# Optimization experiments

Measured on AMD Instinct MI355X. Metric: run time of the kernel, lower is better.

Reference implementation:

```python
import jax, jax.numpy as jnp
import numpy as np
import math


def _packet_loss_to_partial_patch(x, loss_rate):
    # Zero out randomly-chosen 1472-byte chunks of the NHWC-flattened tensor,
    # exactly mirroring the torch loop but as one vectorized masked multiply.
    B, C, H, W = x.shape
    xp = jnp.transpose(x, (0, 2, 3, 1)).reshape(-1)  # NHWC flatten
    n = xp.shape[0]
    elem_size = 4  # float32 bytes
    elems_per_chunk = 1472 // elem_size  # 368
    num_chunks = math.ceil(n * elem_size / 1472)
    num_lossy = int(math.ceil(num_chunks * (loss_rate / 100)))
    perm = jax.random.permutation(jax.random.key(1234), num_chunks)
    keep = jnp.ones((num_chunks,), xp.dtype).at[perm[:num_lossy]].set(0.0)
    elem_keep = jnp.repeat(keep, elems_per_chunk)[:n]
    xp = xp * elem_keep
    return jnp.transpose(xp.reshape(B, H, W, C), (0, 3, 1, 2))


def setup_inputs() -> dict:
    key = jax.random.key(0)
    ks = jax.random.split(key, 7)
    B, C, H, W = 32, 256, 56, 56
    r = 16
    s = 0.05
    return {
        "x": jax.random.normal(ks[0], (B, C, H, W), jnp.float32),
        "fc1_w": jax.random.normal(ks[1], (C // r, C), jnp.float32) * s,
        "fc2_w": jax.random.normal(ks[2], (C, C // r), jnp.float32) * s,
        "threshold": jnp.array([0.5], jnp.float32),
        "detect_w": jax.random.normal(ks[3], (C, C), jnp.float32) * s,
        "rec1_w": jax.random.normal(ks[4], (C, 2 * C), jnp.float32) * s,
        "rec2_w": jax.random.normal(ks[5], (C, C), jnp.float32) * s,
        "adapt_w": jax.random.normal(ks[6], (C, 1), jnp.float32) * s,
        "Packet_Loss_Rate": 50,
    }


def reference(x, fc1_w, fc2_w, threshold, detect_w, rec1_w, rec2_w, adapt_w, Packet_Loss_Rate):
    x = _packet_loss_to_partial_patch(x, Packet_Loss_Rate)
    B, C, H, W = x.shape
    # SE channel attention
    y = jnp.mean(x, axis=(2, 3))                              # [B, C]
    scores = jax.nn.sigmoid(jax.nn.relu(y @ fc1_w.T) @ fc2_w.T)  # [B, C]
    # packet-loss adaptation: Linear(1 -> C) applied to rate*ones([B,1])
    adapt = jnp.asarray(Packet_Loss_Rate, x.dtype) * adapt_w[:, 0]  # [C]
    mask = jax.nn.relu(scores + adapt[None, :] - threshold)   # [B, C]
    mask = mask[:, :, None, None]
    # 1x1 convs as channel GEMMs
    det = jnp.einsum('oc,bchw->bohw', detect_w, x)
    z = jnp.concatenate([x, jax.nn.sigmoid(det) * x], axis=1)  # [B, 2C, H, W]
    r = jax.nn.relu(jnp.einsum('oc,bchw->bohw', rec1_w, z))
    r = jnp.einsum('oc,bchw->bohw', rec2_w, r)
    return r * mask
```

## Files before the change

### kernel.cpp

```cpp
#include <hip/hip_runtime.h>
#include <stdint.h>

#define PARTITIONABLE 1

typedef float f32x4 __attribute__((ext_vector_type(4)));
typedef short bf16x8 __attribute__((ext_vector_type(8)));

namespace {
constexpr int Hh = 56, Ww = 56;
constexpr int HW = Hh * Ww;
constexpr int Bsz = 32, Cch = 256;
constexpr int NCH = 69811;
constexpr int HALF = 34906;
constexpr int NB2 = 4096;

constexpr int SC1_W   = 0;
constexpr int SC2_W   = 139648;
constexpr int BITS1_W = 279296;
constexpr int BITS2_W = 349120;
constexpr int R1_W    = 418944;
constexpr int R2_W    = 488768;
constexpr int HIST1_W = 558592;
constexpr int PRE1_W  = 562688;
constexpr int CNT1_W  = 566784;
constexpr int HIST2_W = 570880;
constexpr int PRE2_W  = 574976;
constexpr int CNT2_W  = 579072;
constexpr int Y_W     = 583168;

constexpr int KEEP_W  = 0;
constexpr int MASKV_W = 69824;
constexpr int WPACK_W = 78016;
}

__host__ __device__ constexpr uint32_t rotl32(uint32_t v, int r) {
  return (v << r) | (v >> (32 - r));
}
__host__ __device__ constexpr uint64_t tf2x32(uint32_t k0, uint32_t k1,
                                              uint32_t x0, uint32_t x1) {
  uint32_t ks2 = k0 ^ k1 ^ 0x1BD11BDAu;
  x0 += k0; x1 += k1;
  {const int R[4]={13,15,26,6};  for(int i=0;i<4;i++){x0+=x1;x1=rotl32(x1,R[i]);x1^=x0;}}
  x0 += k1;  x1 += ks2 + 1u;
  {const int R[4]={17,29,16,24}; for(int i=0;i<4;i++){x0+=x1;x1=rotl32(x1,R[i]);x1^=x0;}}
  x0 += ks2; x1 += k0 + 2u;
  {const int R[4]={13,15,26,6};  for(int i=0;i<4;i++){x0+=x1;x1=rotl32(x1,R[i]);x1^=x0;}}
  x0 += k0;  x1 += k1 + 3u;
  {const int R[4]={17,29,16,24}; for(int i=0;i<4;i++){x0+=x1;x1=rotl32(x1,R[i]);x1^=x0;}}
  x0 += k1;  x1 += ks2 + 4u;
  {const int R[4]={13,15,26,6};  for(int i=0;i<4;i++){x0+=x1;x1=rotl32(x1,R[i]);x1^=x0;}}
  x0 += ks2; x1 += k0 + 5u;
  return ((uint64_t)x0 << 32) | x1;
}

#if PARTITIONABLE
constexpr uint64_t KEY1 = tf2x32(0u, 1234u, 0u, 0u);
constexpr uint64_t SUB1 = tf2x32(0u, 1234u, 0u, 1u);
constexpr uint64_t SUB2 = tf2x32((uint32_t)(KEY1 >> 32), (uint32_t)KEY1, 0u, 1u);
constexpr uint32_t S1H = (uint32_t)(SUB1 >> 32), S1L = (uint32_t)SUB1;
constexpr uint32_t S2H = (uint32_t)(SUB2 >> 32), S2L = (uint32_t)SUB2;
#else
constexpr uint64_t E0 = tf2x32(0u, 1234u, 0u, 2u);
constexpr uint64_t E1 = tf2x32(0u, 1234u, 1u, 3u);
constexpr uint32_t K1H = (uint32_t)(E0 >> 32), K1L = (uint32_t)(E1 >> 32);
constexpr uint64_t F0 = tf2x32(K1H, K1L, 0u, 2u);
constexpr uint64_t F1 = tf2x32(K1H, K1L, 1u, 3u);
constexpr uint32_t S1H = (uint32_t)E0, S1L = (uint32_t)E1;
constexpr uint32_t S2H = (uint32_t)F0, S2L = (uint32_t)F1;
#endif

__device__ __forceinline__ uint32_t rnd_bits(uint32_t kh, uint32_t kl, uint32_t i) {
#if PARTITIONABLE
  uint64_t r = tf2x32(kh, kl, 0u, i);
  return (uint32_t)(r >> 32) ^ (uint32_t)r;
#else
  if (i < (uint32_t)HALF) {
    uint32_t x1 = (i + HALF < (uint32_t)NCH) ? i + HALF : 0u;
    return (uint32_t)(tf2x32(kh, kl, i, x1) >> 32);
  } else {
    return (uint32_t)tf2x32(kh, kl, i - HALF, i);
  }
#endif
}

__device__ __forceinline__ uint32_t f2bf(float f) {
  uint32_t u = __float_as_uint(f);
  return (u + 0x7FFFu + ((u >> 16) & 1u)) >> 16;
}
__device__ __forceinline__ float bf2f(uint32_t h) {
  return __uint_as_float(h << 16);
}
__device__ __forceinline__ uint32_t cvtpk(float lo, float hi) {
  uint32_t r;
  asm("v_cvt_pk_bf16_f32 %0, %1, %2" : "=v"(r) : "v"(lo), "v"(hi));
  return r;
}

__global__ void k_bits(uint32_t* bits1, uint32_t* bits2,
                       uint32_t* hist1, uint32_t* hist2) {
  int i = blockIdx.x * 256 + threadIdx.x;
  if (i >= NCH) return;
  uint32_t b1 = rnd_bits(S1H, S1L, (uint32_t)i);
  uint32_t b2 = rnd_bits(S2H, S2L, (uint32_t)i);
  bits1[i] = b1; bits2[i] = b2;
  atomicAdd(&hist1[b1 >> 20], 1u);
  atomicAdd(&hist2[b2 >> 20], 1u);
}

__global__ __launch_bounds__(1024) void k_scan2(const uint32_t* h1, uint32_t* p1o,
                                                const uint32_t* h2, uint32_t* p2o) {
  const uint32_t* h = blockIdx.x ? h2 : h1;
  uint32_t* pre = blockIdx.x ? p2o : p1o;
  __shared__ uint32_t part[1024];
  int t = threadIdx.x;
  uint4 v = *(const uint4*)&h[t * 4];
  uint32_t s = v.x + v.y + v.z + v.w;
  part[t] = s;
  __syncthreads();
  for (int off = 1; off < 1024; off <<= 1) {
    uint32_t u = (t >= off) ? part[t - off] : 0u;
    __syncthreads();
    part[t] += u;
    __syncthreads();
  }
  uint32_t run = part[t] - s;
  uint4 o;
  o.x = run; o.y = run + v.x; o.z = o.y + v.y; o.w = o.z + v.z;
  *(uint4*)&pre[t * 4] = o;
}

__global__ void k_scatter2(const uint32_t* bits1, const uint32_t* pre1,
                           uint32_t* cnt1, uint64_t* sc1,
                           const uint32_t* bits2, const uint32_t* pre2,
                           uint32_t* cnt2, uint64_t* sc2) {
  int blk = blockIdx.x;
  bool second = blk >= 273;
  const uint32_t* bits = second ? bits2 : bits1;
  const uint32_t* pre  = second ? pre2  : pre1;
  uint32_t* cnt = second ? cnt2 : cnt1;
  uint64_t* sc  = second ? sc2  : sc1;
  int i = (second ? blk - 273 : blk) * 256 + threadIdx.x;
  if (i >= NCH) return;
  uint32_t b = bits[i], bk = b >> 20;
  uint32_t pos = pre[bk] + atomicAdd(&cnt[bk], 1u);
  sc[pos] = ((uint64_t)b << 32) | (uint32_t)i;
}

__global__ void k_rank2(const uint32_t* bits1, const uint32_t* pre1,
                        const uint32_t* hist1, const uint64_t* sc1, uint32_t* rk1,
                        const uint32_t* bits2, const uint32_t* pre2,
                        const uint32_t* hist2, const uint64_t* sc2, uint32_t* rk2) {
  int blk = blockIdx.x;
  bool second = blk >= 273;
  const uint32_t* bits = second ? bits2 : bits1;
  const uint32_t* pre  = second ? pre2  : pre1;
  const uint32_t* hist = second ? hist2 : hist1;
  const uint64_t* sc   = second ? sc2   : sc1;
  uint32_t* rnk = second ? rk2 : rk1;
  int i = (second ? blk - 273 : blk) * 256 + threadIdx.x;
  if (i >= NCH) return;
  uint32_t b = bits[i], bk = b >> 20;
  uint32_t s = pre[bk], n = hist[bk];
  uint64_t my = ((uint64_t)b << 32) | (uint32_t)i;
  uint32_t c = 0;
  for (uint32_t k = 0; k < n; ++k) c += (sc[s + k] < my) ? 1u : 0u;
  rnk[i] = s + c;
}

__global__ void k_keepwpack(const uint32_t* r1, const uint32_t* r2,
                            const int* plr, float* keep,
                            const float* __restrict__ dw,
                            const float* __restrict__ r1w,
                            const float* __restrict__ r2w,
                            ushort* __restrict__ wdp, ushort* __restrict__ w1p,
                            ushort* __restrict__ w2p) {
  int blk = blockIdx.x;
  if (blk < 273) {
    int j = blk * 256 + threadIdx.x;
    if (j >= NCH) return;
    int L = (NCH * plr[0] + 99) / 100;
    keep[j] = (r2[r1[j]] < (uint32_t)L) ? 0.f : 1.f;
    return;
  }
  int tid = (blk - 273) * 256 + threadIdx.x;
  const float* src;
  ushort* dst;
  if (tid < 8192) {
    int s = tid, ot = s >> 9, ks = (s >> 6) & 7, l = s & 63;
    src = dw + (ot * 16 + (l & 15)) * 256 + ks * 32 + (l >> 4) * 8;
    dst = wdp + s * 8;
  } else if (tid < 24576) {
    int s = tid - 8192, ot = s >> 10, ks = (s >> 6) & 15, l = s & 63;
    src = r1w + (ot * 16 + (l & 15)) * 512 + ks * 32 + (l >> 4) * 8;
    dst = w1p + s * 8;
  } else {
    int s = tid - 24576, ot = s >> 9, ks = (s >> 6) & 7, l = s & 63;
    src = r2w + (ot * 16 + (l & 15)) * 256 + ks * 32 + (l >> 4) * 8;
    dst = w2p + s * 8;
  }
  float4 v0 = *(const float4*)src;
  float4 v1 = *(const float4*)(src + 4);
  uint4 pk;
  pk.x = f2bf(v0.x) | (f2bf(v0.y) << 16);
  pk.y = f2bf(v0.z) | (f2bf(v0.w) << 16);
  pk.z = f2bf(v1.x) | (f2bf(v1.y) << 16);
  pk.w = f2bf(v1.z) | (f2bf(v1.w) << 16);
  *(uint4*)dst = pk;
}

__global__ void k_ymean(const float* __restrict__ x, const float* __restrict__ keep,
                        float* __restrict__ y) {
  int bc = blockIdx.x;
  int b = bc >> 8, c = bc & 255;
  const float4* row = (const float4*)(x + (size_t)bc * HW);
  int t = threadIdx.x;
  float s = 0.f;
  for (int q = t; q < HW / 4; q += 256) {
    float4 v = row[q];
    uint32_t base = (uint32_t)((b * HW + q * 4) * 256 + c);
    s += v.x * keep[base / 368u];
    s += v.y * keep[(base + 256u) / 368u];
    s += v.z * keep[(base + 512u) / 368u];
    s += v.w * keep[(base + 768u) / 368u];
  }
  for (int off = 32; off > 0; off >>= 1) s += __shfl_down(s, off);
  __shared__ float w4[4];
  if ((t & 63) == 0) w4[t >> 6] = s;
  __syncthreads();
  if (t == 0) y[bc] = (w4[0] + w4[1] + w4[2] + w4[3]) * (1.0f / HW);
}

__global__ void k_scores(const float* __restrict__ y, const float* __restrict__ fc1,
                         const float* __restrict__ fc2, const float* __restrict__ thr,
                         const float* __restrict__ aw, const int* __restrict__ plr,
                         float* __restrict__ maskv) {
  int b = blockIdx.x, t = threadIdx.x;
  __shared__ float ysh[256];
  __shared__ float hsh[16];
  ysh[t] = y[b * 256 + t];
  __syncthreads();
  if (t < 16) {
    float a = 0.f;
    for (int c = 0; c < 256; ++c) a += ysh[c] * fc1[t * 256 + c];
    hsh[t] = fmaxf(a, 0.f);
  }
  __syncthreads();
  float s = 0.f;
  #pragma unroll
  for (int j = 0; j < 16; ++j) s += hsh[j] * fc2[t * 16 + j];
  float sc = 1.f / (1.f + expf(-s));
  float m = sc + (float)plr[0] * aw[t] - thr[0];
  maskv[b * 256 + t] = fmaxf(m, 0.f);
}

__global__ __launch_bounds__(1024, 8) void k_main(
    const float* __restrict__ x, const float* __restrict__ keep,
    const ushort* __restrict__ wdp, const ushort* __restrict__ w1p,
    const ushort* __restrict__ w2p, const float* __restrict__ maskv,
    float* __restrict__ out) {
  __shared__ __align__(16) short SM[32768];
  int tile = blockIdx.x;
  int bb = tile / 49, hw0 = (tile % 49) * 64;
  int t = threadIdx.x;
  int lane = t & 63, w = t >> 6;
  int l15 = lane & 15, lhi = lane >> 4;

  {
    const float* xb = x + (size_t)bb * (Cch * HW);
    uint32_t pixb = (uint32_t)(bb * HW + hw0);
    int p = lane;
    uint32_t ia0 = (pixb + (uint32_t)p) * 256u;
    uint32_t k0 = ia0 / 368u;
    uint32_t cstar = 368u * (k0 + 1u) - ia0;
    float kp0 = keep[k0];
    float kp1 = keep[k0 + 1];
    const float* xcol = xb + hw0 + p;
    int ks = w >> 1;
    #pragma unroll
    for (int k2 = 0; k2 < 2; ++k2) {
      int k = (w & 1) * 2 + k2;
      int cb = ks * 32 + k * 8;
      uint32_t pw[4];
      #pragma unroll
      for (int h = 0; h < 4; ++h) {
        uint32_t ca = (uint32_t)(cb + h * 2);
        float va = xcol[(size_t)ca * HW] * (ca < cstar ? kp0 : kp1);
        float vb = xcol[(size_t)(ca + 1u) * HW] * ((ca + 1u) < cstar ? kp0 : kp1);
        pw[h] = cvtpk(va, vb);
      }
      uint4 pk; pk.x = pw[0]; pk.y = pw[1]; pk.z = pw[2]; pk.w = pw[3];
      *(uint4*)&SM[(ks * 4 + (p >> 4)) * 512 + ((p & 15) + 16 * k) * 8] = pk;
    }
  }
  __syncthreads();

  f32x4 zero4 = {0.f, 0.f, 0.f, 0.f};
  f32x4 acc[4];
  int stoff = ((w >> 1) * 4) * 512 +
              (l15 + 16 * ((w & 1) * 2 + (lhi >> 1))) * 8 + (lhi & 1) * 4;

  #pragma unroll
  for (int nt = 0; nt < 4; ++nt) acc[nt] = zero4;
  {
    const ushort* ap = wdp + (w * 8) * 512 + lane * 8;
    bf16x8 a0 = *(const bf16x8*)ap;
    #pragma unroll
    for (int ks = 0; ks < 8; ++ks) {
      bf16x8 na0 = a0;
      if (ks < 7) na0 = *(const bf16x8*)(ap + (ks + 1) * 512);
      #pragma unroll
      for (int nt = 0; nt < 4; ++nt) {
        bf16x8 b = *(const bf16x8*)&SM[(ks * 4 + nt) * 512 + lane * 8];
        acc[nt] = __builtin_amdgcn_mfma_f32_16x16x32_bf16(a0, b, acc[nt], 0, 0, 0);
      }
      a0 = na0;
    }
  }

  #pragma unroll
  for (int nt = 0; nt < 4; ++nt) {
    int off = stoff + nt * 512;
    ushort4 xv = *(const ushort4*)&SM[off];
    float s0 = bf2f(xv.x) / (1.f + __expf(-acc[nt][0]));
    float s1 = bf2f(xv.y) / (1.f + __expf(-acc[nt][1]));
    float s2 = bf2f(xv.z) / (1.f + __expf(-acc[nt][2]));
    float s3 = bf2f(xv.w) / (1.f + __expf(-acc[nt][3]));
    uint2 sv;
    sv.x = cvtpk(s0, s1);
    sv.y = cvtpk(s2, s3);
    *(uint2*)&SM[16384 + off] = sv;
  }
  __syncthreads();

  f32x4 acc2[4];
  #pragma unroll
  for (int nt = 0; nt < 4; ++nt) acc2[nt] = zero4;
  {
    const ushort* ap = w1p + (w * 16) * 512 + lane * 8;
    bf16x8 a0 = *(const bf16x8*)ap;
    #pragma unroll
    for (int ks = 0; ks < 16; ++ks) {
      bf16x8 na0 = a0;
      if (ks < 15) na0 = *(const bf16x8*)(ap + (ks + 1) * 512);
      #pragma unroll
      for (int nt = 0; nt < 4; ++nt) {
        bf16x8 b = *(const bf16x8*)&SM[(ks * 4 + nt) * 512 + lane * 8];
        acc2[nt] = __builtin_amdgcn_mfma_f32_16x16x32_bf16(a0, b, acc2[nt], 0, 0, 0);
      }
      a0 = na0;
    }
  }
  __syncthreads();

  #pragma unroll
  for (int nt = 0; nt < 4; ++nt) {
    int off = stoff + nt * 512;
    uint2 rv;
    rv.x = cvtpk(fmaxf(acc2[nt][0], 0.f), fmaxf(acc2[nt][1], 0.f));
    rv.y = cvtpk(fmaxf(acc2[nt][2], 0.f), fmaxf(acc2[nt][3], 0.f));
    *(uint2*)&SM[off] = rv;
  }
  __syncthreads();

  #pragma unroll
  for (int nt = 0; nt < 4; ++nt) acc[nt] = zero4;
  {
    const ushort* ap = w2p + (w * 8) * 512 + lane * 8;
    bf16x8 a0 = *(const bf16x8*)ap;
    #pragma unroll
    for (int ks = 0; ks < 8; ++ks) {
      bf16x8 na0 = a0;
      if (ks < 7) na0 = *(const bf16x8*)(ap + (ks + 1) * 512);
      #pragma unroll
      for (int nt = 0; nt < 4; ++nt) {
        bf16x8 b = *(const bf16x8*)&SM[(ks * 4 + nt) * 512 + lane * 8];
        acc[nt] = __builtin_amdgcn_mfma_f32_16x16x32_bf16(a0, b, acc[nt], 0, 0, 0);
      }
      a0 = na0;
    }
  }
  __syncthreads();

  {
    float* EP = (float*)SM;
    int sw = ((lhi & 1) << 2) | ((lhi >> 1) << 4);
    #pragma unroll
    for (int r = 0; r < 4; ++r) {
      int c = w * 16 + 4 * lhi + r;
      float m = maskv[bb * 256 + c];
      #pragma unroll
      for (int nt = 0; nt < 4; ++nt)
        EP[c * 64 + ((nt * 16 + l15) ^ sw)] = acc[nt][r] * m;
    }
  }
  __syncthreads();
  {
    const float* EP = (const float*)SM;
    float* op = out + (size_t)bb * (Cch * HW) + hw0;
    #pragma unroll
    for (int q = 0; q < 4; ++q) {
      int idx4 = q * 1024 + t;
      int c = idx4 >> 4;
      int colw = (idx4 & 15) * 4;
      int p = colw ^ ((((c >> 2) & 1) << 2) | (((c >> 3) & 1) << 4));
      f32x4 v = *(const f32x4*)&EP[idx4 * 4];
      *(f32x4*)(op + (size_t)c * HW + p) = v;
    }
  }
}

extern "C" void kernel_launch(void* const* d_in, const int* in_sizes, int n_in,
                              void* d_out, int out_size, void* d_ws, size_t ws_size,
                              hipStream_t stream) {
  const float* x   = (const float*)d_in[0];
  const float* fc1 = (const float*)d_in[1];
  const float* fc2 = (const float*)d_in[2];
  const float* thr = (const float*)d_in[3];
  const float* dw  = (const float*)d_in[4];
  const float* r1w = (const float*)d_in[5];
  const float* r2w = (const float*)d_in[6];
  const float* aw  = (const float*)d_in[7];
  const int*   plr = (const int*)d_in[8];

  float*    out = (float*)d_out;
  uint32_t* ob  = (uint32_t*)d_out;
  float*    ws  = (float*)d_ws;

  uint64_t* sc1   = (uint64_t*)(ob + SC1_W);
  uint64_t* sc2   = (uint64_t*)(ob + SC2_W);
  uint32_t* bits1 = ob + BITS1_W;
  uint32_t* bits2 = ob + BITS2_W;
  uint32_t* r1    = ob + R1_W;
  uint32_t* r2    = ob + R2_W;
  uint32_t* hist1 = ob + HIST1_W;
  uint32_t* pre1  = ob + PRE1_W;
  uint32_t* cnt1  = ob + CNT1_W;
  uint32_t* hist2 = ob + HIST2_W;
  uint32_t* pre2  = ob + PRE2_W;
  uint32_t* cnt2  = ob + CNT2_W;
  float*    yv    = (float*)(ob + Y_W);

  float*  keep  = ws + KEEP_W;
  float*  maskv = ws + MASKV_W;
  ushort* wdp   = (ushort*)(ws + WPACK_W);
  ushort* w1p   = wdp + 65536;
  ushort* w2p   = w1p + 131072;

  hipMemsetAsync((void*)(ob + HIST1_W), 0, (size_t)6 * NB2 * 4, stream);

  dim3 blk(256);
  k_bits<<<273, blk, 0, stream>>>(bits1, bits2, hist1, hist2);
  k_scan2<<<2, 1024, 0, stream>>>(hist1, pre1, hist2, pre2);
  k_scatter2<<<546, blk, 0, stream>>>(bits1, pre1, cnt1, sc1,
                                      bits2, pre2, cnt2, sc2);
  k_rank2<<<546, blk, 0, stream>>>(bits1, pre1, hist1, sc1, r1,
                                   bits2, pre2, hist2, sc2, r2);
  k_keepwpack<<<401, blk, 0, stream>>>(r1, r2, plr, keep, dw, r1w, r2w,
                                       wdp, w1p, w2p);
  k_ymean<<<8192, blk, 0, stream>>>(x, keep, yv);
  k_scores<<<32, blk, 0, stream>>>(yv, fc1, fc2, thr, aw, plr, maskv);
  k_main<<<1568, 1024, 0, stream>>>(x, keep, wdp, w1p, w2p, maskv, out);
}
```

Measured before the change: 158.5 us.

## Switch fused GEMM chain to 32x32x16 MFMA with 256-thread blocks

Repacks the three weight matrices for the 32x32x16 bf16 MFMA layout and rewrites the main kernel so each of 4 waves computes a 64-channel by 64-pixel tile as 2x2 32x32 MFMA blocks, instead of 16 waves each doing 16x16 tiles. Fewer waves load more weight fragments each and reuse every LDS B fragment across two MFMAs. The aim is higher arithmetic per LDS read and less weight traffic per block. In exchange each wave holds far more accumulator registers, so occupancy and latency hiding drop. The epilogue also loses its LDS swizzle, which can add bank conflicts.

Result: slower. 178.3 us (+12.5%).

```diff
diff --git a/kernel.cpp b/kernel.cpp
--- a/kernel.cpp
+++ b/kernel.cpp
@@ -4,6 +4,7 @@
 #define PARTITIONABLE 1
 
 typedef float f32x4 __attribute__((ext_vector_type(4)));
+typedef float f32x16 __attribute__((ext_vector_type(16)));
 typedef short bf16x8 __attribute__((ext_vector_type(8)));
 
 namespace {
@@ -186,16 +187,16 @@
   const float* src;
   ushort* dst;
   if (tid < 8192) {
-    int s = tid, ot = s >> 9, ks = (s >> 6) & 7, l = s & 63;
-    src = dw + (ot * 16 + (l & 15)) * 256 + ks * 32 + (l >> 4) * 8;
+    int s = tid, ct = s >> 10, ks = (s >> 6) & 15, l = s & 63;
+    src = dw + (ct * 32 + (l & 31)) * 256 + ks * 16 + (l >> 5) * 8;
     dst = wdp + s * 8;
   } else if (tid < 24576) {
-    int s = tid - 8192, ot = s >> 10, ks = (s >> 6) & 15, l = s & 63;
-    src = r1w + (ot * 16 + (l & 15)) * 512 + ks * 32 + (l >> 4) * 8;
+    int s = tid - 8192, ct = s >> 11, ks = (s >> 6) & 31, l = s & 63;
+    src = r1w + (ct * 32 + (l & 31)) * 512 + ks * 16 + (l >> 5) * 8;
     dst = w1p + s * 8;
   } else {
-    int s = tid - 24576, ot = s >> 9, ks = (s >> 6) & 7, l = s & 63;
-    src = r2w + (ot * 16 + (l & 15)) * 256 + ks * 32 + (l >> 4) * 8;
+    int s = tid - 24576, ct = s >> 10, ks = (s >> 6) & 15, l = s & 63;
+    src = r2w + (ct * 32 + (l & 31)) * 256 + ks * 16 + (l >> 5) * 8;
     dst = w2p + s * 8;
   }
   float4 v0 = *(const float4*)src;
@@ -253,7 +254,7 @@
   maskv[b * 256 + t] = fmaxf(m, 0.f);
 }
 
-__global__ __launch_bounds__(1024, 8) void k_main(
+__global__ __launch_bounds__(256, 2) void k_main(
     const float* __restrict__ x, const float* __restrict__ keep,
     const ushort* __restrict__ wdp, const ushort* __restrict__ w1p,
     const ushort* __restrict__ w2p, const float* __restrict__ maskv,
@@ -263,134 +264,175 @@
   int bb = tile / 49, hw0 = (tile % 49) * 64;
   int t = threadIdx.x;
   int lane = t & 63, w = t >> 6;
-  int l15 = lane & 15, lhi = lane >> 4;
+  int l31 = lane & 31, lhi = lane >> 5;
 
   {
-    const float* xb = x + (size_t)bb * (Cch * HW);
-    uint32_t pixb = (uint32_t)(bb * HW + hw0);
-    int p = lane;
-    uint32_t ia0 = (pixb + (uint32_t)p) * 256u;
+    int px = t & 63;
+    uint32_t ia0 = (uint32_t)(bb * HW + hw0 + px) * 256u;
     uint32_t k0 = ia0 / 368u;
     uint32_t cstar = 368u * (k0 + 1u) - ia0;
-    float kp0 = keep[k0];
-    float kp1 = keep[k0 + 1];
-    const float* xcol = xb + hw0 + p;
-    int ks = w >> 1;
-    #pragma unroll
-    for (int k2 = 0; k2 < 2; ++k2) {
-      int k = (w & 1) * 2 + k2;
-      int cb = ks * 32 + k * 8;
+    float kp0 = keep[k0], kp1 = keep[k0 + 1];
+    const float* xcol = x + (size_t)bb * (Cch * HW) + hw0 + px;
+    int g0 = t >> 6;
+    int nt = px >> 5;
+    float xr[8][8];
+    #pragma unroll
+    for (int gi = 0; gi < 8; ++gi) {
+      int cb = g0 * 8 + gi * 32;
+      #pragma unroll
+      for (int h = 0; h < 8; ++h)
+        xr[gi][h] = xcol[(size_t)(cb + h) * HW];
+    }
+    #pragma unroll
+    for (int gi = 0; gi < 8; ++gi) {
+      int G = g0 + gi * 4;
+      int cb = G * 8;
       uint32_t pw[4];
       #pragma unroll
       for (int h = 0; h < 4; ++h) {
-        uint32_t ca = (uint32_t)(cb + h * 2);
-        float va = xcol[(size_t)ca * HW] * (ca < cstar ? kp0 : kp1);
-        float vb = xcol[(size_t)(ca + 1u) * HW] * ((ca + 1u) < cstar ? kp0 : kp1);
+        uint32_t ca = (uint32_t)(cb + 2 * h);
+        float va = xr[gi][2 * h]     * (ca < cstar ? kp0 : kp1);
+        float vb = xr[gi][2 * h + 1] * ((ca + 1u) < cstar ? kp0 : kp1);
         pw[h] = cvtpk(va, vb);
       }
       uint4 pk; pk.x = pw[0]; pk.y = pw[1]; pk.z = pw[2]; pk.w = pw[3];
-      *(uint4*)&SM[(ks * 4 + (p >> 4)) * 512 + ((p & 15) + 16 * k) * 8] = pk;
-    }
-  }
-  __syncthreads();
-
-  f32x4 zero4 = {0.f, 0.f, 0.f, 0.f};
-  f32x4 acc[4];
-  int stoff = ((w >> 1) * 4) * 512 +
-              (l15 + 16 * ((w & 1) * 2 + (lhi >> 1))) * 8 + (lhi & 1) * 4;
+      int ks = G >> 1, half = G & 1;
+      *(uint4*)&SM[(((ks * 2 + nt) * 64) + half * 32 + (px & 31)) * 8] = pk;
+    }
+  }
+  __syncthreads();
+
+  const f32x16 z16 = {0.f};
+  f32x16 acc[2][2];
+
+  acc[0][0] = z16; acc[0][1] = z16; acc[1][0] = z16; acc[1][1] = z16;
+  {
+    const ushort* a0p = wdp + (size_t)(w * 2 + 0) * 16 * 512 + lane * 8;
+    const ushort* a1p = a0p + 16 * 512;
+    bf16x8 a0 = *(const bf16x8*)a0p;
+    bf16x8 a1 = *(const bf16x8*)a1p;
+    #pragma unroll
+    for (int ks = 0; ks < 16; ++ks) {
+      bf16x8 na0 = a0, na1 = a1;
+      if (ks < 15) {
+        na0 = *(const bf16x8*)(a0p + (ks + 1) * 512);
+        na1 = *(const bf16x8*)(a1p + (ks + 1) * 512);
+      }
+      #pragma unroll
+      for (int nt = 0; nt < 2; ++nt) {
+        bf16x8 b = *(const bf16x8*)&SM[(ks * 2 + nt) * 512 + lane * 8];
+        acc[0][nt] = __builtin_amdgcn_mfma_f32_32x32x16_bf16(a0, b, acc[0][nt], 0, 0, 0);
+        acc[1][nt] = __builtin_amdgcn_mfma_f32_32x32x16_bf16(a1, b, acc[1][nt], 0, 0, 0);
+      }
+      a0 = na0; a1 = na1;
+    }
+  }
 
   #pragma unroll
-  for (int nt = 0; nt < 4; ++nt) acc[nt] = zero4;
+  for (int tc = 0; tc < 2; ++tc) {
+    #pragma unroll
+    for (int q = 0; q < 4; ++q) {
+      int ksp = (w * 2 + tc) * 2 + (q >> 1);
+      int dl = ((q & 1) << 5) | l31;
+      #pragma unroll
+      for (int nt = 0; nt < 2; ++nt) {
+        int base = (ksp * 2 + nt) * 512 + dl * 8 + lhi * 4;
+        ushort4 xv = *(const ushort4*)&SM[base];
+        float e0 = bf2f(xv.x) / (1.f + __expf(-acc[tc][nt][4 * q + 0]));
+        float e1 = bf2f(xv.y) / (1.f + __expf(-acc[tc][nt][4 * q + 1]));
+        float e2 = bf2f(xv.z) / (1.f + __expf(-acc[tc][nt][4 * q + 2]));
+        float e3 = bf2f(xv.w) / (1.f + __expf(-acc[tc][nt][4 * q + 3]));
+        uint2 sv;
+        sv.x = cvtpk(e0, e1);
+        sv.y = cvtpk(e2, e3);
+        *(uint2*)&SM[16384 + base] = sv;
+      }
+    }
+  }
+  __syncthreads();
+
+  f32x16 acc2[2][2];
+  acc2[0][0] = z16; acc2[0][1] = z16; acc2[1][0] = z16; acc2[1][1] = z16;
   {
-    const ushort* ap = wdp + (w * 8) * 512 + lane * 8;
-    bf16x8 a0 = *(const bf16x8*)ap;
-    #pragma unroll
-    for (int ks = 0; ks < 8; ++ks) {
-      bf16x8 na0 = a0;
-      if (ks < 7) na0 = *(const bf16x8*)(ap + (ks + 1) * 512);
-      #pragma unroll
-      for (int nt = 0; nt < 4; ++nt) {
-        bf16x8 b = *(const bf16x8*)&SM[(ks * 4 + nt) * 512 + lane * 8];
-        acc[nt] = __builtin_amdgcn_mfma_f32_16x16x32_bf16(a0, b, acc[nt], 0, 0, 0);
-      }
-      a0 = na0;
-    }
-  }
+    const ushort* a0p = w1p + (size_t)(w * 2 + 0) * 32 * 512 + lane * 8;
+    const ushort* a1p = a0p + 32 * 512;
+    bf16x8 a0 = *(const bf16x8*)a0p;
+    bf16x8 a1 = *(const bf16x8*)a1p;
+    #pragma unroll
+    for (int ks = 0; ks < 32; ++ks) {
+      bf16x8 na0 = a0, na1 = a1;
+      if (ks < 31) {
+        na0 = *(const bf16x8*)(a0p + (ks + 1) * 512);
+        na1 = *(const bf16x8*)(a1p + (ks + 1) * 512);
+      }
+      #pragma unroll
+      for (int nt = 0; nt < 2; ++nt) {
+        bf16x8 b = *(const bf16x8*)&SM[(ks * 2 + nt) * 512 + lane * 8];
+        acc2[0][nt] = __builtin_amdgcn_mfma_f32_32x32x16_bf16(a0, b, acc2[0][nt], 0, 0, 0);
+        acc2[1][nt] = __builtin_amdgcn_mfma_f32_32x32x16_bf16(a1, b, acc2[1][nt], 0, 0, 0);
+      }
+      a0 = na0; a1 = na1;
+    }
+  }
+  __syncthreads();
 
   #pragma unroll
-  for (int nt = 0; nt < 4; ++nt) {
-    int off = stoff + nt * 512;
-    ushort4 xv = *(const ushort4*)&SM[off];
-    float s0 = bf2f(xv.x) / (1.f + __expf(-acc[nt][0]));
-    float s1 = bf2f(xv.y) / (1.f + __expf(-acc[nt][1]));
-    float s2 = bf2f(xv.z) / (1.f + __expf(-acc[nt][2]));
-    float s3 = bf2f(xv.w) / (1.f + __expf(-acc[nt][3]));
-    uint2 sv;
-    sv.x = cvtpk(s0, s1);
-    sv.y = cvtpk(s2, s3);
-    *(uint2*)&SM[16384 + off] = sv;
-  }
-  __syncthreads();
-
-  f32x4 acc2[4];
-  #pragma unroll
-  for (int nt = 0; nt < 4; ++nt) acc2[nt] = zero4;
+  for (int tc = 0; tc < 2; ++tc) {
+    #pragma unroll
+    for (int q = 0; q < 4; ++q) {
+      int ksp = (w * 2 + tc) * 2 + (q >> 1);
+      int dl = ((q & 1) << 5) | l31;
+      #pragma unroll
+      for (int nt = 0; nt < 2; ++nt) {
+        int base = (ksp * 2 + nt) * 512 + dl * 8 + lhi * 4;
+        uint2 rv;
+        rv.x = cvtpk(fmaxf(acc2[tc][nt][4 * q + 0], 0.f),
+                     fmaxf(acc2[tc][nt][4 * q + 1], 0.f));
+        rv.y = cvtpk(fmaxf(acc2[tc][nt][4 * q + 2], 0.f),
+                     fmaxf(acc2[tc][nt][4 * q + 3], 0.f));
+        *(uint2*)&SM[base] = rv;
+      }
+    }
+  }
+  __syncthreads();
+
+  acc[0][0] = z16; acc[0][1] = z16; acc[1][0] = z16; acc[1][1] = z16;
   {
-    const ushort* ap = w1p + (w * 16) * 512 + lane * 8;
-    bf16x8 a0 = *(const bf16x8*)ap;
+    const ushort* a0p = w2p + (size_t)(w * 2 + 0) * 16 * 512 + lane * 8;
+    const ushort* a1p = a0p + 16 * 512;
+    bf16x8 a0 = *(const bf16x8*)a0p;
+    bf16x8 a1 = *(const bf16x8*)a1p;
     #pragma unroll
     for (int ks = 0; ks < 16; ++ks) {
-      bf16x8 na0 = a0;
-      if (ks < 15) na0 = *(const bf16x8*)(ap + (ks + 1) * 512);
-      #pragma unroll
-      for (int nt = 0; nt < 4; ++nt) {
-        bf16x8 b = *(const bf16x8*)&SM[(ks * 4 + nt) * 512 + lane * 8];
-        acc2[nt] = __builtin_amdgcn_mfma_f32_16x16x32_bf16(a0, b, acc2[nt], 0, 0, 0);
-      }
-      a0 = na0;
-    }
-  }
-  __syncthreads();
-
-  #pragma unroll
-  for (int nt = 0; nt < 4; ++nt) {
-    int off = stoff + nt * 512;
-    uint2 rv;
-    rv.x = cvtpk(fmaxf(acc2[nt][0], 0.f), fmaxf(acc2[nt][1], 0.f));
-    rv.y = cvtpk(fmaxf(acc2[nt][2], 0.f), fmaxf(acc2[nt][3], 0.f));
-    *(uint2*)&SM[off] = rv;
-  }
-  __syncthreads();
-
-  #pragma unroll
-  for (int nt = 0; nt < 4; ++nt) acc[nt] = zero4;
-  {
-    const ushort* ap = w2p + (w * 8) * 512 + lane * 8;
-    bf16x8 a0 = *(const bf16x8*)ap;
-    #pragma unroll
-    for (int ks = 0; ks < 8; ++ks) {
-      bf16x8 na0 = a0;
-      if (ks < 7) na0 = *(const bf16x8*)(ap + (ks + 1) * 512);
-      #pragma unroll
-      for (int nt = 0; nt < 4; ++nt) {
-        bf16x8 b = *(const bf16x8*)&SM[(ks * 4 + nt) * 512 + lane * 8];
-        acc[nt] = __builtin_amdgcn_mfma_f32_16x16x32_bf16(a0, b, acc[nt], 0, 0, 0);
-      }
-      a0 = na0;
+      bf16x8 na0 = a0, na1 = a1;
+      if (ks < 15) {
+        na0 = *(const bf16x8*)(a0p + (ks + 1) * 512);
+        na1 = *(const bf16x8*)(a1p + (ks + 1) * 512);
+      }
+      #pragma unroll
+      for (int nt = 0; nt < 2; ++nt) {
+        bf16x8 b = *(const bf16x8*)&SM[(ks * 2 + nt) * 512 + lane * 8];
+        acc[0][nt] = __builtin_amdgcn_mfma_f32_32x32x16_bf16(a0, b, acc[0][nt], 0, 0, 0);
+        acc[1][nt] = __builtin_amdgcn_mfma_f32_32x32x16_bf16(a1, b, acc[1][nt], 0, 0, 0);
+      }
+      a0 = na0; a1 = na1;
     }
   }
   __syncthreads();
 
   {
     float* EP = (float*)SM;
-    int sw = ((lhi & 1) << 2) | ((lhi >> 1) << 4);
-    #pragma unroll
-    for (int r = 0; r < 4; ++r) {
-      int c = w * 16 + 4 * lhi + r;
-      float m = maskv[bb * 256 + c];
-      #pragma unroll
-      for (int nt = 0; nt < 4; ++nt)
-        EP[c * 64 + ((nt * 16 + l15) ^ sw)] = acc[nt][r] * m;
+    #pragma unroll
+    for (int tc = 0; tc < 2; ++tc) {
+      #pragma unroll
+      for (int r = 0; r < 16; ++r) {
+        int row = (r & 3) + 8 * (r >> 2) + 4 * lhi;
+        int ch = (w * 2 + tc) * 32 + row;
+        float m = maskv[bb * 256 + ch];
+        #pragma unroll
+        for (int nt = 0; nt < 2; ++nt)
+          EP[ch * 64 + nt * 32 + l31] = acc[tc][nt][r] * m;
+      }
     }
   }
   __syncthreads();
@@ -398,13 +440,11 @@
     const float* EP = (const float*)SM;
     float* op = out + (size_t)bb * (Cch * HW) + hw0;
     #pragma unroll
-    for (int q = 0; q < 4; ++q) {
-      int idx4 = q * 1024 + t;
-      int c = idx4 >> 4;
-      int colw = (idx4 & 15) * 4;
-      int p = colw ^ ((((c >> 2) & 1) << 2) | (((c >> 3) & 1) << 4));
-      f32x4 v = *(const f32x4*)&EP[idx4 * 4];
-      *(f32x4*)(op + (size_t)c * HW + p) = v;
+    for (int q = 0; q < 16; ++q) {
+      int chunk = q * 256 + t;
+      int ch = chunk >> 4, p4 = (chunk & 15) * 4;
+      f32x4 v = *(const f32x4*)&EP[chunk * 4];
+      *(f32x4*)(op + (size_t)ch * HW + p4) = v;
     }
   }
 }
@@ -459,5 +499,5 @@
                                        wdp, w1p, w2p);
   k_ymean<<<8192, blk, 0, stream>>>(x, keep, yv);
   k_scores<<<32, blk, 0, stream>>>(yv, fc1, fc2, thr, aw, plr, maskv);
-  k_main<<<1568, 1024, 0, stream>>>(x, keep, wdp, w1p, w2p, maskv, out);
-}
+  k_main<<<1568, 256, 0, stream>>>(x, keep, wdp, w1p, w2p, maskv, out);
+}
```
